# Kernel optimization log

Measured on AMD Instinct MI355X. Metric: run time of the kernel, lower is better.

Reference implementation:

```python
import jax, jax.numpy as jnp
import numpy as np

C = 256          # simi channels (hardcoded in source)
HM = 128         # feature map spatial size (clamps to 127 in source)
OH = 11          # simi_size_h = int(88/8)
OW = 8           # simi_size   = int(66/8)
MARGIN = 0.1


def setup_inputs() -> dict:
    key = jax.random.key(0)
    ks = jax.random.split(key, 6)
    B, Nf, Nm = 8, 4, 2
    simi = jax.random.normal(ks[0], (B, C, HM, HM), jnp.float32)
    hm = jax.random.normal(ks[1], (B, 1, HM, HM), jnp.float32)
    hm_gt = jax.random.uniform(ks[2], (B, 1, HM, HM), jnp.float32) * 0.9
    hm_gt = hm_gt.at[:, :, ::32, ::32].set(1.0)  # sparse positive centers

    def mk_boxes(k, n):
        k1, k2, k3, k4 = jax.random.split(k, 4)
        x0 = jax.random.randint(k1, (B, n), 0, 96)
        y0 = jax.random.randint(k2, (B, n), 0, 96)
        w = jax.random.randint(k3, (B, n), 8, 30)
        h = jax.random.randint(k4, (B, n), 8, 30)
        return jnp.stack([x0, y0, jnp.minimum(x0 + w, 127), jnp.minimum(y0 + h, 127)], -1).astype(jnp.int32)

    bboxf = mk_boxes(ks[3], Nf)
    bboxm = mk_boxes(ks[4], Nm)
    gamma = jnp.ones((C,), jnp.float32)
    beta = jnp.zeros((C,), jnp.float32)
    return dict(simi=simi, hm=hm, hm_gt=hm_gt, bboxf=bboxf, bboxm=bboxm, gamma=gamma, beta=beta)


def _crop_resize(img_all, bidx, box):
    # Faithful to: slice simi_hm[b,:,y0:y1,x0:x1] then F.interpolate(..., [11,8], 'bilinear')
    # (align_corners=False). Implemented as direct bilinear sampling into the full map.
    x0, y0, x1, y1 = box[0], box[1], box[2], box[3]
    h = (y1 - y0).astype(jnp.float32)
    w = (x1 - x0).astype(jnp.float32)
    sy = jnp.clip((jnp.arange(OH, dtype=jnp.float32) + 0.5) * h / OH - 0.5, 0.0, h - 1.0)
    sx = jnp.clip((jnp.arange(OW, dtype=jnp.float32) + 0.5) * w / OW - 0.5, 0.0, w - 1.0)
    ylo = jnp.floor(sy).astype(jnp.int32)
    xlo = jnp.floor(sx).astype(jnp.int32)
    yhi = jnp.minimum(ylo + 1, y1 - y0 - 1)
    xhi = jnp.minimum(xlo + 1, x1 - x0 - 1)
    wy = sy - ylo
    wx = sx - xlo
    img = img_all[bidx]                       # [C, 128, 128]
    ya, yb = y0 + ylo, y0 + yhi
    xa, xb = x0 + xlo, x0 + xhi
    v00 = img[:, ya[:, None], xa[None, :]]    # [C, 11, 8]
    v01 = img[:, ya[:, None], xb[None, :]]
    v10 = img[:, yb[:, None], xa[None, :]]
    v11 = img[:, yb[:, None], xb[None, :]]
    top = (1.0 - wx) * v00 + wx * v01
    bot = (1.0 - wx) * v10 + wx * v11
    out = (1.0 - wy)[:, None] * top + wy[:, None] * bot
    return out.reshape(-1)                    # flatten in C,H,W order like torch.flatten


_crop_all = jax.vmap(_crop_resize, in_axes=(None, 0, 0))


def _focal_loss(pred, gt):
    # CenterNet focal loss
    pos = (gt == 1.0).astype(pred.dtype)
    neg = 1.0 - pos
    neg_w = jnp.power(1.0 - gt, 4)
    pos_loss = jnp.log(pred) * jnp.square(1.0 - pred) * pos
    neg_loss = jnp.log(1.0 - pred) * jnp.square(pred) * neg_w * neg
    num_pos = pos.sum()
    return -(pos_loss.sum() + neg_loss.sum()) / jnp.maximum(num_pos, 1.0)


def _pdist(a, b):
    # torch PairwiseDistance(2): ||a - b + eps||_2, eps=1e-6
    return jnp.sqrt(jnp.sum(jnp.square(a - b + 1e-6), axis=-1))


def reference(simi, hm, hm_gt, bboxf, bboxm, gamma, beta):
    # BatchNorm2d in training mode (fresh module: batch stats, biased var, eps=1e-5)
    mean = simi.mean((0, 2, 3), keepdims=True)
    var = simi.var((0, 2, 3), keepdims=True)
    simi_n = (simi - mean) / jnp.sqrt(var + 1e-5) * gamma[None, :, None, None] + beta[None, :, None, None]

    B, Nf = bboxf.shape[0], bboxf.shape[1]
    Nm = bboxm.shape[1]
    bidx_f = jnp.repeat(jnp.arange(B), Nf)
    bidx_m = jnp.repeat(jnp.arange(B), Nm)
    faces = _crop_all(simi_n, bidx_f, bboxf.reshape(-1, 4))   # [B*Nf, C*OH*OW]
    masks = _crop_all(simi_n, bidx_m, bboxm.reshape(-1, 4))   # [B*Nm, C*OH*OW]

    total_f = faces.shape[0]
    half = total_f // 2
    # with total_m == total_f//2, match_size == total_m and no random re-fill branch fires
    anchor = faces[:half]
    positive = faces[half:total_f]
    negative = masks
    pos_dist = _pdist(anchor, positive)
    neg_dist = _pdist(anchor, negative)
    triplet = jnp.mean(jnp.maximum(MARGIN + pos_dist - neg_dist, 0.0))

    pred_hm = jnp.clip(jax.nn.sigmoid(hm), 1e-4, 1.0 - 1e-4)  # _sigmoid
    hm_loss = _focal_loss(pred_hm, hm_gt)
    return hm_loss + triplet
```

## Files before the change

kernel.cpp:

```cpp
#include <hip/hip_runtime.h>
#include <math.h>

#define CCH 256
#define HMD 128
#define HW (HMD*HMD)
#define NTOT (8*HW)
#define OH 11
#define OW 8
#define NPIX (OH*OW)
#define NPAIR 16

#define CH_SUM 0
#define CH_SQ  2048
#define TRI    4096
#define FOC    20480

__device__ __forceinline__ void block_reduce2(float& a, float& b) {
    #pragma unroll
    for (int off = 32; off > 0; off >>= 1) {
        a += __shfl_down(a, off, 64);
        b += __shfl_down(b, off, 64);
    }
    __shared__ float sa[4], sb[4];
    int wid  = threadIdx.x >> 6;
    int lane = threadIdx.x & 63;
    if (lane == 0) { sa[wid] = a; sb[wid] = b; }
    __syncthreads();
    if (threadIdx.x == 0) {
        a = sa[0] + sa[1] + sa[2] + sa[3];
        b = sb[0] + sb[1] + sb[2] + sb[3];
    }
}

__global__ void mega(const float* __restrict__ simi,
                     const float* __restrict__ hm,
                     const float* __restrict__ gt,
                     const int* __restrict__ bboxf,
                     const int* __restrict__ bboxm,
                     float* __restrict__ ws) {
    const int bid = blockIdx.x;
    const int tid = threadIdx.x;

    if (bid < 128) {
        int pair  = bid >> 3;
        int slice = bid & 7;

        __shared__ int   sYA[3][OH], sYB[3][OH], sXA[3][OW], sXB[3][OW];
        __shared__ float sWY[3][OH], sWX[3][OW];
        __shared__ int   sBase[3];

        if (tid < 3) {
            const int* bx;
            int bidx;
            if (tid == 0)      { bx = bboxf + pair * 4;        bidx = pair >> 2; }
            else if (tid == 1) { bx = bboxf + (16 + pair) * 4; bidx = 4 + (pair >> 2); }
            else               { bx = bboxm + pair * 4;        bidx = pair >> 1; }
            int x0 = bx[0], y0 = bx[1], x1 = bx[2], y1 = bx[3];
            float h = (float)(y1 - y0), w = (float)(x1 - x0);
            for (int j = 0; j < OH; ++j) {
                float sy = fminf(fmaxf((j + 0.5f) * h / (float)OH - 0.5f, 0.0f), h - 1.0f);
                int ylo = (int)floorf(sy);
                sYA[tid][j] = y0 + ylo;
                sYB[tid][j] = y0 + min(ylo + 1, y1 - y0 - 1);
                sWY[tid][j] = sy - (float)ylo;
            }
            for (int j = 0; j < OW; ++j) {
                float sx = fminf(fmaxf((j + 0.5f) * w / (float)OW - 0.5f, 0.0f), w - 1.0f);
                int xlo = (int)floorf(sx);
                sXA[tid][j] = x0 + xlo;
                sXB[tid][j] = x0 + min(xlo + 1, x1 - x0 - 1);
                sWX[tid][j] = sx - (float)xlo;
            }
            sBase[tid] = bidx * CCH * HW;
        }
        __syncthreads();

        int cl = tid >> 3;
        int lx = tid & 7;
        int c  = slice * 32 + cl;

        const float* imgA = simi + sBase[0] + c * HW;
        const float* imgP = simi + sBase[1] + c * HW;
        const float* imgN = simi + sBase[2] + c * HW;

        float a1p = 0.f, a2p = 0.f, a1n = 0.f, a2n = 0.f;
        float wxA = sWX[0][lx], wxP = sWX[1][lx], wxN = sWX[2][lx];
        int xaA = sXA[0][lx], xbA = sXB[0][lx];
        int xaP = sXA[1][lx], xbP = sXB[1][lx];
        int xaN = sXA[2][lx], xbN = sXB[2][lx];

        #pragma unroll
        for (int y = 0; y < OH; ++y) {
            float wyA = sWY[0][y], wyP = sWY[1][y], wyN = sWY[2][y];
            int yaA = sYA[0][y] * HMD, ybA = sYB[0][y] * HMD;
            int yaP = sYA[1][y] * HMD, ybP = sYB[1][y] * HMD;
            int yaN = sYA[2][y] * HMD, ybN = sYB[2][y] * HMD;

            float vA, vP, vN;
            {
                float v00 = imgA[yaA + xaA], v01 = imgA[yaA + xbA];
                float v10 = imgA[ybA + xaA], v11 = imgA[ybA + xbA];
                float top = (1.0f - wxA) * v00 + wxA * v01;
                float bot = (1.0f - wxA) * v10 + wxA * v11;
                vA = (1.0f - wyA) * top + wyA * bot;
            }
            {
                float v00 = imgP[yaP + xaP], v01 = imgP[yaP + xbP];
                float v10 = imgP[ybP + xaP], v11 = imgP[ybP + xbP];
                float top = (1.0f - wxP) * v00 + wxP * v01;
                float bot = (1.0f - wxP) * v10 + wxP * v11;
                vP = (1.0f - wyP) * top + wyP * bot;
            }
            {
                float v00 = imgN[yaN + xaN], v01 = imgN[yaN + xbN];
                float v10 = imgN[ybN + xaN], v11 = imgN[ybN + xbN];
                float top = (1.0f - wxN) * v00 + wxN * v01;
                float bot = (1.0f - wxN) * v10 + wxN * v11;
                vN = (1.0f - wyN) * top + wyN * bot;
            }
            float dp = vA - vP; a1p += dp; a2p += dp * dp;
            float dn = vA - vN; a1n += dn; a2n += dn * dn;
        }
        #pragma unroll
        for (int off = 4; off > 0; off >>= 1) {
            a1p += __shfl_down(a1p, off, 8);
            a2p += __shfl_down(a2p, off, 8);
            a1n += __shfl_down(a1n, off, 8);
            a2n += __shfl_down(a2n, off, 8);
        }
        if (lx == 0) {
            float* q = ws + TRI + (pair * 256 + c) * 4;
            q[0] = a1p; q[1] = a2p; q[2] = a1n; q[3] = a2n;
        }
    } else if (bid < 256) {
        int f = bid - 128;
        int i = f * 256 + tid;
        float4 hv = ((const float4*)hm)[i];
        float4 gv = ((const float4*)gt)[i];
        float lsum = 0.f, npos = 0.f;
        #pragma unroll
        for (int j = 0; j < 4; ++j) {
            float x = (&hv.x)[j], g = (&gv.x)[j];
            float pred = 1.0f / (1.0f + expf(-x));
            pred = fminf(fmaxf(pred, 1e-4f), 1.0f - 1e-4f);
            if (g == 1.0f) {
                float om = 1.0f - pred;
                lsum += logf(pred) * om * om;
                npos += 1.0f;
            } else {
                float gg = 1.0f - g;
                float g2 = gg * gg;
                lsum += logf(1.0f - pred) * pred * pred * (g2 * g2);
            }
        }
        block_reduce2(lsum, npos);
        if (tid == 0) { ws[FOC + 2 * f] = lsum; ws[FOC + 2 * f + 1] = npos; }
    } else {
        int p = bid - 256;
        const float4* p4 = (const float4*)(simi + (size_t)p * HW);
        float s = 0.f, s2 = 0.f;
        #pragma unroll
        for (int it = 0; it < 16; ++it) {
            float4 v = p4[it * 256 + tid];
            s  += v.x + v.y + v.z + v.w;
            s2 += v.x*v.x + v.y*v.y + v.z*v.z + v.w*v.w;
        }
        block_reduce2(s, s2);
        if (tid == 0) { ws[CH_SUM + p] = s; ws[CH_SQ + p] = s2; }
    }
}

__global__ void finalize(const float* __restrict__ ws,
                         const float* __restrict__ gamma,
                         float* __restrict__ out) {
    __shared__ float s_sh[256], tr[NPAIR];
    int t = threadIdx.x;

    float su = 0.f, sq = 0.f;
    #pragma unroll
    for (int b = 0; b < 8; ++b) {
        su += ws[CH_SUM + b * 256 + t];
        sq += ws[CH_SQ  + b * 256 + t];
    }
    const float invn = 1.0f / (float)NTOT;
    float mean = su * invn;
    float var  = sq * invn - mean * mean;
    s_sh[t] = gamma[t] / sqrtf(var + 1e-5f);
    __syncthreads();

    int pair = t >> 4, cl = t & 15;
    float pdl = 0.f, ndl = 0.f;
    #pragma unroll
    for (int k = 0; k < 16; ++k) {
        int c = cl + 16 * k;
        float s = s_sh[c];
        const float* q = ws + TRI + (pair * 256 + c) * 4;
        pdl += s * s * q[1] + 2e-6f * s * q[0];
        ndl += s * s * q[3] + 2e-6f * s * q[2];
    }
    #pragma unroll
    for (int off = 8; off > 0; off >>= 1) {
        pdl += __shfl_down(pdl, off, 16);
        ndl += __shfl_down(ndl, off, 16);
    }
    if (cl == 0) {
        const float e2 = 1e-12f * (float)(CCH * NPIX);
        tr[pair] = fmaxf(0.1f + sqrtf(pdl + e2) - sqrtf(ndl + e2), 0.0f);
    }

    float l = 0.f, np = 0.f;
    if (t < 128) { l = ws[FOC + 2 * t]; np = ws[FOC + 2 * t + 1]; }
    block_reduce2(l, np);

    if (t == 0) {
        float trip = 0.f;
        #pragma unroll
        for (int p = 0; p < NPAIR; ++p) trip += tr[p];
        trip *= (1.0f / (float)NPAIR);
        out[0] = -l / fmaxf(np, 1.0f) + trip;
    }
}

extern "C" void kernel_launch(void* const* d_in, const int* in_sizes, int n_in,
                              void* d_out, int out_size, void* d_ws, size_t ws_size,
                              hipStream_t stream) {
    const float* simi  = (const float*)d_in[0];
    const float* hm    = (const float*)d_in[1];
    const float* hm_gt = (const float*)d_in[2];
    const int*   bboxf = (const int*)d_in[3];
    const int*   bboxm = (const int*)d_in[4];
    const float* gamma = (const float*)d_in[5];
    float* out = (float*)d_out;
    float* ws  = (float*)d_ws;

    mega<<<2304, 256, 0, stream>>>(simi, hm, hm_gt, bboxf, bboxm, ws);
    finalize<<<1, 256, 0, stream>>>(ws, gamma, out);
}
```

Measured before the change: 34.83 us.

## Move bilinear gather after streaming pass and fold finalize into last block

Splits the work so the streaming channel-statistics and focal-loss blocks run first, then a second 128-block kernel does the bilinear gathers, likely hitting cache lines the stream pass just pulled in. The separate finalize kernel is removed: an atomic counter reset in the first kernel picks the last-finishing gather block to do the final reduction. This targets the gather blocks' scattered global-memory latency and one kernel launch. It adds threadfence and atomic overhead, and the 128 gather blocks now run alone rather than overlapping with the streaming blocks.

After: 42.52 us. +22.1%, slower.

```diff
diff --git a/kernel.cpp b/kernel.cpp
--- a/kernel.cpp
+++ b/kernel.cpp
@@ -14,6 +14,7 @@
 #define CH_SQ  2048
 #define TRI    4096
 #define FOC    20480
+#define CNT    20736
 
 __device__ __forceinline__ void block_reduce2(float& a, float& b) {
     #pragma unroll
@@ -32,109 +33,17 @@
     }
 }
 
-__global__ void mega(const float* __restrict__ simi,
-                     const float* __restrict__ hm,
-                     const float* __restrict__ gt,
-                     const int* __restrict__ bboxf,
-                     const int* __restrict__ bboxm,
-                     float* __restrict__ ws) {
+__global__ void stream_pass(const float* __restrict__ simi,
+                            const float* __restrict__ hm,
+                            const float* __restrict__ gt,
+                            float* __restrict__ ws) {
     const int bid = blockIdx.x;
     const int tid = threadIdx.x;
 
+    if (bid == 0 && tid == 0) ((unsigned int*)ws)[CNT] = 0u;
+
     if (bid < 128) {
-        int pair  = bid >> 3;
-        int slice = bid & 7;
-
-        __shared__ int   sYA[3][OH], sYB[3][OH], sXA[3][OW], sXB[3][OW];
-        __shared__ float sWY[3][OH], sWX[3][OW];
-        __shared__ int   sBase[3];
-
-        if (tid < 3) {
-            const int* bx;
-            int bidx;
-            if (tid == 0)      { bx = bboxf + pair * 4;        bidx = pair >> 2; }
-            else if (tid == 1) { bx = bboxf + (16 + pair) * 4; bidx = 4 + (pair >> 2); }
-            else               { bx = bboxm + pair * 4;        bidx = pair >> 1; }
-            int x0 = bx[0], y0 = bx[1], x1 = bx[2], y1 = bx[3];
-            float h = (float)(y1 - y0), w = (float)(x1 - x0);
-            for (int j = 0; j < OH; ++j) {
-                float sy = fminf(fmaxf((j + 0.5f) * h / (float)OH - 0.5f, 0.0f), h - 1.0f);
-                int ylo = (int)floorf(sy);
-                sYA[tid][j] = y0 + ylo;
-                sYB[tid][j] = y0 + min(ylo + 1, y1 - y0 - 1);
-                sWY[tid][j] = sy - (float)ylo;
-            }
-            for (int j = 0; j < OW; ++j) {
-                float sx = fminf(fmaxf((j + 0.5f) * w / (float)OW - 0.5f, 0.0f), w - 1.0f);
-                int xlo = (int)floorf(sx);
-                sXA[tid][j] = x0 + xlo;
-                sXB[tid][j] = x0 + min(xlo + 1, x1 - x0 - 1);
-                sWX[tid][j] = sx - (float)xlo;
-            }
-            sBase[tid] = bidx * CCH * HW;
-        }
-        __syncthreads();
-
-        int cl = tid >> 3;
-        int lx = tid & 7;
-        int c  = slice * 32 + cl;
-
-        const float* imgA = simi + sBase[0] + c * HW;
-        const float* imgP = simi + sBase[1] + c * HW;
-        const float* imgN = simi + sBase[2] + c * HW;
-
-        float a1p = 0.f, a2p = 0.f, a1n = 0.f, a2n = 0.f;
-        float wxA = sWX[0][lx], wxP = sWX[1][lx], wxN = sWX[2][lx];
-        int xaA = sXA[0][lx], xbA = sXB[0][lx];
-        int xaP = sXA[1][lx], xbP = sXB[1][lx];
-        int xaN = sXA[2][lx], xbN = sXB[2][lx];
-
-        #pragma unroll
-        for (int y = 0; y < OH; ++y) {
-            float wyA = sWY[0][y], wyP = sWY[1][y], wyN = sWY[2][y];
-            int yaA = sYA[0][y] * HMD, ybA = sYB[0][y] * HMD;
-            int yaP = sYA[1][y] * HMD, ybP = sYB[1][y] * HMD;
-            int yaN = sYA[2][y] * HMD, ybN = sYB[2][y] * HMD;
-
-            float vA, vP, vN;
-            {
-                float v00 = imgA[yaA + xaA], v01 = imgA[yaA + xbA];
-                float v10 = imgA[ybA + xaA], v11 = imgA[ybA + xbA];
-                float top = (1.0f - wxA) * v00 + wxA * v01;
-                float bot = (1.0f - wxA) * v10 + wxA * v11;
-                vA = (1.0f - wyA) * top + wyA * bot;
-            }
-            {
-                float v00 = imgP[yaP + xaP], v01 = imgP[yaP + xbP];
-                float v10 = imgP[ybP + xaP], v11 = imgP[ybP + xbP];
-                float top = (1.0f - wxP) * v00 + wxP * v01;
-                float bot = (1.0f - wxP) * v10 + wxP * v11;
-                vP = (1.0f - wyP) * top + wyP * bot;
-            }
-            {
-                float v00 = imgN[yaN + xaN], v01 = imgN[yaN + xbN];
-                float v10 = imgN[ybN + xaN], v11 = imgN[ybN + xbN];
-                float top = (1.0f - wxN) * v00 + wxN * v01;
-                float bot = (1.0f - wxN) * v10 + wxN * v11;
-                vN = (1.0f - wyN) * top + wyN * bot;
-            }
-            float dp = vA - vP; a1p += dp; a2p += dp * dp;
-            float dn = vA - vN; a1n += dn; a2n += dn * dn;
-        }
-        #pragma unroll
-        for (int off = 4; off > 0; off >>= 1) {
-            a1p += __shfl_down(a1p, off, 8);
-            a2p += __shfl_down(a2p, off, 8);
-            a1n += __shfl_down(a1n, off, 8);
-            a2n += __shfl_down(a2n, off, 8);
-        }
-        if (lx == 0) {
-            float* q = ws + TRI + (pair * 256 + c) * 4;
-            q[0] = a1p; q[1] = a2p; q[2] = a1n; q[3] = a2n;
-        }
-    } else if (bid < 256) {
-        int f = bid - 128;
-        int i = f * 256 + tid;
+        int i = bid * 256 + tid;
         float4 hv = ((const float4*)hm)[i];
         float4 gv = ((const float4*)gt)[i];
         float lsum = 0.f, npos = 0.f;
@@ -154,9 +63,9 @@
             }
         }
         block_reduce2(lsum, npos);
-        if (tid == 0) { ws[FOC + 2 * f] = lsum; ws[FOC + 2 * f + 1] = npos; }
+        if (tid == 0) { ws[FOC + 2 * bid] = lsum; ws[FOC + 2 * bid + 1] = npos; }
     } else {
-        int p = bid - 256;
+        int p = bid - 128;
         const float4* p4 = (const float4*)(simi + (size_t)p * HW);
         float s = 0.f, s2 = 0.f;
         #pragma unroll
@@ -170,11 +79,118 @@
     }
 }
 
-__global__ void finalize(const float* __restrict__ ws,
-                         const float* __restrict__ gamma,
-                         float* __restrict__ out) {
+__global__ void gather_finalize(const float* __restrict__ simi,
+                                const int* __restrict__ bboxf,
+                                const int* __restrict__ bboxm,
+                                const float* __restrict__ gamma,
+                                float* __restrict__ ws,
+                                float* __restrict__ out) {
+    const int bid = blockIdx.x;
+    const int tid = threadIdx.x;
+    int pair  = bid >> 3;
+    int slice = bid & 7;
+
+    __shared__ int   sYA[3][OH], sYB[3][OH], sXA[3][OW], sXB[3][OW];
+    __shared__ float sWY[3][OH], sWX[3][OW];
+    __shared__ int   sBase[3];
+
+    if (tid < 3) {
+        const int* bx;
+        int bidx;
+        if (tid == 0)      { bx = bboxf + pair * 4;        bidx = pair >> 2; }
+        else if (tid == 1) { bx = bboxf + (16 + pair) * 4; bidx = 4 + (pair >> 2); }
+        else               { bx = bboxm + pair * 4;        bidx = pair >> 1; }
+        int x0 = bx[0], y0 = bx[1], x1 = bx[2], y1 = bx[3];
+        float h = (float)(y1 - y0), w = (float)(x1 - x0);
+        for (int j = 0; j < OH; ++j) {
+            float sy = fminf(fmaxf((j + 0.5f) * h / (float)OH - 0.5f, 0.0f), h - 1.0f);
+            int ylo = (int)floorf(sy);
+            sYA[tid][j] = y0 + ylo;
+            sYB[tid][j] = y0 + min(ylo + 1, y1 - y0 - 1);
+            sWY[tid][j] = sy - (float)ylo;
+        }
+        for (int j = 0; j < OW; ++j) {
+            float sx = fminf(fmaxf((j + 0.5f) * w / (float)OW - 0.5f, 0.0f), w - 1.0f);
+            int xlo = (int)floorf(sx);
+            sXA[tid][j] = x0 + xlo;
+            sXB[tid][j] = x0 + min(xlo + 1, x1 - x0 - 1);
+            sWX[tid][j] = sx - (float)xlo;
+        }
+        sBase[tid] = bidx * CCH * HW;
+    }
+    __syncthreads();
+
+    int cl = tid >> 3;
+    int lx = tid & 7;
+    int c  = slice * 32 + cl;
+
+    const float* imgA = simi + sBase[0] + c * HW;
+    const float* imgP = simi + sBase[1] + c * HW;
+    const float* imgN = simi + sBase[2] + c * HW;
+
+    float a1p = 0.f, a2p = 0.f, a1n = 0.f, a2n = 0.f;
+    float wxA = sWX[0][lx], wxP = sWX[1][lx], wxN = sWX[2][lx];
+    int xaA = sXA[0][lx], xbA = sXB[0][lx];
+    int xaP = sXA[1][lx], xbP = sXB[1][lx];
+    int xaN = sXA[2][lx], xbN = sXB[2][lx];
+
+    #pragma unroll
+    for (int y = 0; y < OH; ++y) {
+        float wyA = sWY[0][y], wyP = sWY[1][y], wyN = sWY[2][y];
+        int yaA = sYA[0][y] * HMD, ybA = sYB[0][y] * HMD;
+        int yaP = sYA[1][y] * HMD, ybP = sYB[1][y] * HMD;
+        int yaN = sYA[2][y] * HMD, ybN = sYB[2][y] * HMD;
+
+        float vA, vP, vN;
+        {
+            float v00 = imgA[yaA + xaA], v01 = imgA[yaA + xbA];
+            float v10 = imgA[ybA + xaA], v11 = imgA[ybA + xbA];
+            float top = (1.0f - wxA) * v00 + wxA * v01;
+            float bot = (1.0f - wxA) * v10 + wxA * v11;
+            vA = (1.0f - wyA) * top + wyA * bot;
+        }
+        {
+            float v00 = imgP[yaP + xaP], v01 = imgP[yaP + xbP];
+            float v10 = imgP[ybP + xaP], v11 = imgP[ybP + xbP];
+            float top = (1.0f - wxP) * v00 + wxP * v01;
+            float bot = (1.0f - wxP) * v10 + wxP * v11;
+            vP = (1.0f - wyP) * top + wyP * bot;
+        }
+        {
+            float v00 = imgN[yaN + xaN], v01 = imgN[yaN + xbN];
+            float v10 = imgN[ybN + xaN], v11 = imgN[ybN + xbN];
+            float top = (1.0f - wxN) * v00 + wxN * v01;
+            float bot = (1.0f - wxN) * v10 + wxN * v11;
+            vN = (1.0f - wyN) * top + wyN * bot;
+        }
+        float dp = vA - vP; a1p += dp; a2p += dp * dp;
+        float dn = vA - vN; a1n += dn; a2n += dn * dn;
+    }
+    #pragma unroll
+    for (int off = 4; off > 0; off >>= 1) {
+        a1p += __shfl_down(a1p, off, 8);
+        a2p += __shfl_down(a2p, off, 8);
+        a1n += __shfl_down(a1n, off, 8);
+        a2n += __shfl_down(a2n, off, 8);
+    }
+    if (lx == 0) {
+        float* q = ws + TRI + (pair * 256 + c) * 4;
+        q[0] = a1p; q[1] = a2p; q[2] = a1n; q[3] = a2n;
+    }
+
+    __shared__ int sLast;
+    __syncthreads();
+    if (tid == 0) {
+        __threadfence();
+        unsigned int old = atomicAdd((unsigned int*)ws + CNT, 1u);
+        sLast = (old == 127u) ? 1 : 0;
+    }
+    __syncthreads();
+    if (!sLast) return;
+    __threadfence();
+
     __shared__ float s_sh[256], tr[NPAIR];
-    int t = threadIdx.x;
+    int t = tid;
 
     float su = 0.f, sq = 0.f;
     #pragma unroll
@@ -188,13 +204,13 @@
     s_sh[t] = gamma[t] / sqrtf(var + 1e-5f);
     __syncthreads();
 
-    int pair = t >> 4, cl = t & 15;
+    int pr = t >> 4, cl2 = t & 15;
     float pdl = 0.f, ndl = 0.f;
     #pragma unroll
     for (int k = 0; k < 16; ++k) {
-        int c = cl + 16 * k;
-        float s = s_sh[c];
-        const float* q = ws + TRI + (pair * 256 + c) * 4;
+        int cc = cl2 + 16 * k;
+        float s = s_sh[cc];
+        const float* q = ws + TRI + (pr * 256 + cc) * 4;
         pdl += s * s * q[1] + 2e-6f * s * q[0];
         ndl += s * s * q[3] + 2e-6f * s * q[2];
     }
@@ -203,9 +219,9 @@
         pdl += __shfl_down(pdl, off, 16);
         ndl += __shfl_down(ndl, off, 16);
     }
-    if (cl == 0) {
+    if (cl2 == 0) {
         const float e2 = 1e-12f * (float)(CCH * NPIX);
-        tr[pair] = fmaxf(0.1f + sqrtf(pdl + e2) - sqrtf(ndl + e2), 0.0f);
+        tr[pr] = fmaxf(0.1f + sqrtf(pdl + e2) - sqrtf(ndl + e2), 0.0f);
     }
 
     float l = 0.f, np = 0.f;
@@ -233,6 +249,6 @@
     float* out = (float*)d_out;
     float* ws  = (float*)d_ws;
 
-    mega<<<2304, 256, 0, stream>>>(simi, hm, hm_gt, bboxf, bboxm, ws);
-    finalize<<<1, 256, 0, stream>>>(ws, gamma, out);
-}
+    stream_pass<<<2176, 256, 0, stream>>>(simi, hm, hm_gt, ws);
+    gather_finalize<<<128, 256, 0, stream>>>(simi, bboxf, bboxm, gamma, ws, out);
+}
```
